# Kernel optimization log

Measured on AMD Instinct MI355X. Metric: run time of the kernel, lower is better.

Reference implementation:

```python
import jax, jax.numpy as jnp
import numpy as np

EMBED = 2048
HEADS = 16
HEAD_DIM = EMBED // HEADS


def setup_inputs() -> dict:
    key = jax.random.key(0)
    ks = jax.random.split(key, 9)
    s = 1.0 / np.sqrt(EMBED)
    inp = {"x": jax.random.normal(ks[0], (2, 2048, EMBED), dtype=jnp.float32)}
    for i, name in enumerate(["q", "k", "v", "o"]):
        inp[f"W{name}"] = jax.random.uniform(ks[1 + 2 * i], (EMBED, EMBED), dtype=jnp.float32, minval=-s, maxval=s)
        inp[f"b{name}"] = jax.random.uniform(ks[2 + 2 * i], (EMBED,), dtype=jnp.float32, minval=-s, maxval=s)
    return inp


def reference(x, Wq, bq, Wk, bk, Wv, bv, Wo, bo):
    B, S, E = x.shape
    def split_heads(t):
        return t.reshape(B, S, HEADS, HEAD_DIM).transpose(0, 2, 1, 3)  # [B,H,S,D]
    q = split_heads(x @ Wq.T + bq)
    k = split_heads(x @ Wk.T + bk)
    v = split_heads(x @ Wv.T + bv)
    scale = 1.0 / np.sqrt(HEAD_DIM)
    scores = jnp.einsum("bhqd,bhkd->bhqk", q, k) * scale  # [B,H,S,S]
    causal = jnp.tril(jnp.ones((S, S), dtype=bool))
    scores = jnp.where(causal[None, None], scores, -jnp.inf)
    attn = jax.nn.softmax(scores, axis=-1)
    out = jnp.einsum("bhqk,bhkd->bhqd", attn, v)  # [B,H,S,D]
    out = out.transpose(0, 2, 1, 3).reshape(B, S, E)
    return out @ Wo.T + bo
```

## Files before the change

kernel.cpp:

```cpp
#include <hip/hip_runtime.h>

typedef unsigned short u16;
typedef unsigned int u32;
typedef __attribute__((ext_vector_type(8))) short bf16x8;
typedef __attribute__((ext_vector_type(4))) float f32x4;

#define MFMA(a, b, c) __builtin_amdgcn_mfma_f32_16x16x32_bf16((a), (b), (c), 0, 0, 0)

__device__ inline u16 f2bf(float f) {
  u32 u = __float_as_uint(f);
  u = (u + 0x7fffu + ((u >> 16) & 1u)) >> 16;
  return (u16)u;
}

__device__ inline void gld16(u16* lds, const u16* g) {
  __builtin_amdgcn_global_load_lds((const __attribute__((address_space(1))) void*)g,
                                   (__attribute__((address_space(3))) void*)lds,
                                   16, 0, 0);
}

__global__ __launch_bounds__(256) void cvt_all(const float* __restrict__ x,
                                               const float* __restrict__ wa,
                                               const float* __restrict__ wb,
                                               const float* __restrict__ wc,
                                               const float* __restrict__ wd,
                                               uint2* __restrict__ dst) {
  int i = blockIdx.x * 256 + threadIdx.x;
  const float* s;
  int off;
  if (i < 2097152) {
    s = x; off = i;
  } else {
    int j = i - 2097152;
    int which = j >> 20;
    off = j & 1048575;
    s = (which == 0) ? wa : (which == 1) ? wb : (which == 2) ? wc : wd;
  }
  float4 f = ((const float4*)s)[off];
  u32 lo = (u32)f2bf(f.x) | ((u32)f2bf(f.y) << 16);
  u32 hi = (u32)f2bf(f.z) | ((u32)f2bf(f.w) << 16);
  dst[i] = make_uint2(lo, hi);
}

__device__ inline void gemm_core(const u16* __restrict__ A, const u16* __restrict__ W,
                                 u16* As, u16* Bs, int m0, int n0, f32x4 acc[4][4]) {
  const int K = 2048;
  const int NT = 64;
  int t = threadIdx.x, w = t >> 6, l = t & 63;
  int wr = (w >> 1) * 64, wc = (w & 1) * 64;
  int fr = l & 15, fg = l >> 4;
  int r0 = t >> 2;
  int r1 = 64 + r0;
  int c00 = (t & 3) ^ ((r0 >> 1) & 3);
  int c01 = (t & 3) ^ ((r1 >> 1) & 3);
  const u16* gA = A + (size_t)m0 * K;
  const u16* gB = W + (size_t)n0 * K;
  size_t a0 = (size_t)r0 * K + c00 * 8;
  size_t a1 = (size_t)r1 * K + c01 * 8;
#pragma unroll
  for (int p = 0; p < 2; ++p) {
    u16* sa = As + p * 4096;
    u16* sb = Bs + p * 4096;
    int kk = p * 32;
    gld16(sa + w * 512, gA + a0 + kk);
    gld16(sa + 2048 + w * 512, gA + a1 + kk);
    gld16(sb + w * 512, gB + a0 + kk);
    gld16(sb + 2048 + w * 512, gB + a1 + kk);
  }
  for (int kt = 0; kt < NT; ++kt) {
    int kt2 = (kt + 2 < NT) ? (kt + 2) : (NT - 1);
    u16* sa = As + ((kt + 2) & 3) * 4096;
    u16* sb = Bs + ((kt + 2) & 3) * 4096;
    int kk = kt2 * 32;
    gld16(sa + w * 512, gA + a0 + kk);
    gld16(sa + 2048 + w * 512, gA + a1 + kk);
    gld16(sb + w * 512, gB + a0 + kk);
    gld16(sb + 2048 + w * 512, gB + a1 + kk);
    asm volatile("s_waitcnt vmcnt(8)\n\ts_barrier" ::: "memory");
    const u16* ca = As + (kt & 3) * 4096;
    const u16* cb = Bs + (kt & 3) * 4096;
    bf16x8 af[4], bfv[4];
#pragma unroll
    for (int i = 0; i < 4; ++i) {
      int ar = wr + i * 16 + fr;
      af[i] = *(const bf16x8*)&ca[ar * 32 + ((fg ^ ((ar >> 1) & 3)) << 3)];
    }
#pragma unroll
    for (int i = 0; i < 4; ++i) {
      int br = wc + i * 16 + fr;
      bfv[i] = *(const bf16x8*)&cb[br * 32 + ((fg ^ ((br >> 1) & 3)) << 3)];
    }
    __builtin_amdgcn_s_setprio(1);
#pragma unroll
    for (int mi = 0; mi < 4; ++mi)
#pragma unroll
      for (int ni = 0; ni < 4; ++ni)
        acc[mi][ni] = MFMA(af[mi], bfv[ni], acc[mi][ni]);
    __builtin_amdgcn_s_setprio(0);
  }
}

__global__ __launch_bounds__(512, 2) void qk_gemm(
    const u16* __restrict__ X, const u16* __restrict__ Wq, const u16* __restrict__ Wk,
    const float* __restrict__ bq, const float* __restrict__ bk, u16* __restrict__ Qo,
    u16* __restrict__ Ko) {
  __shared__ __attribute__((aligned(16))) u16 As[32768];
  __shared__ __attribute__((aligned(16))) u16 Bs[32768];
  const int K = 2048, NT = 64;
  int which = blockIdx.x >> 3;
  int n0 = (blockIdx.x & 7) * 256;
  int m0 = blockIdx.y * 256;
  const u16* W = (which == 0) ? Wq : Wk;
  const float* bias = (which == 0) ? bq : bk;
  u16* out = (which == 0) ? Qo : Ko;
  float scale = (which == 0) ? 0.08838834764831845f : 1.0f;
  int t = threadIdx.x, w = t >> 6, l = t & 63;
  int wm = w >> 2, wn = w & 3;
  int fr = l & 15, fg = l >> 4;
  int r0 = t >> 2;
  int c0 = (t & 3) ^ ((r0 >> 1) & 3);
  const u16* gA = X + (size_t)m0 * K;
  const u16* gB = W + (size_t)n0 * K;
  size_t a0 = (size_t)r0 * K + c0 * 8;
  size_t a1 = a0 + (size_t)128 * K;
  f32x4 zero4 = {0.f, 0.f, 0.f, 0.f};
  f32x4 acc[8][4];
#pragma unroll
  for (int i = 0; i < 8; ++i)
#pragma unroll
    for (int j = 0; j < 4; ++j) acc[i][j] = zero4;
#pragma unroll
  for (int p = 0; p < 2; ++p) {
    u16* sa = As + p * 8192;
    u16* sb = Bs + p * 8192;
    int kk = p * 32;
    gld16(sa + w * 512, gA + a0 + kk);
    gld16(sa + 4096 + w * 512, gA + a1 + kk);
    gld16(sb + w * 512, gB + a0 + kk);
    gld16(sb + 4096 + w * 512, gB + a1 + kk);
  }
  for (int kt = 0; kt < NT; ++kt) {
    int kt2 = (kt + 2 < NT) ? (kt + 2) : (NT - 1);
    u16* sa = As + ((kt + 2) & 3) * 8192;
    u16* sb = Bs + ((kt + 2) & 3) * 8192;
    int kk = kt2 * 32;
    gld16(sa + w * 512, gA + a0 + kk);
    gld16(sa + 4096 + w * 512, gA + a1 + kk);
    gld16(sb + w * 512, gB + a0 + kk);
    gld16(sb + 4096 + w * 512, gB + a1 + kk);
    asm volatile("s_waitcnt vmcnt(8)\n\ts_barrier" ::: "memory");
    const u16* ca = As + (kt & 3) * 8192;
    const u16* cb = Bs + (kt & 3) * 8192;
    bf16x8 af[8], bfv[4];
#pragma unroll
    for (int i = 0; i < 8; ++i) {
      int ar = wm * 128 + i * 16 + fr;
      af[i] = *(const bf16x8*)&ca[ar * 32 + ((fg ^ ((ar >> 1) & 3)) << 3)];
    }
#pragma unroll
    for (int i = 0; i < 4; ++i) {
      int br = wn * 64 + i * 16 + fr;
      bfv[i] = *(const bf16x8*)&cb[br * 32 + ((fg ^ ((br >> 1) & 3)) << 3)];
    }
    __builtin_amdgcn_s_setprio(1);
#pragma unroll
    for (int mi = 0; mi < 8; ++mi)
#pragma unroll
      for (int ni = 0; ni < 4; ++ni)
        acc[mi][ni] = MFMA(af[mi], bfv[ni], acc[mi][ni]);
    __builtin_amdgcn_s_setprio(0);
  }
#pragma unroll
  for (int mi = 0; mi < 8; ++mi) {
#pragma unroll
    for (int ni = 0; ni < 4; ++ni) {
      int row = m0 + wm * 128 + mi * 16 + (l >> 4) * 4;
      int col = n0 + wn * 64 + ni * 16 + (l & 15);
      float bb = bias[col];
      int h = col >> 7, d = col & 127;
#pragma unroll
      for (int i = 0; i < 4; ++i) {
        int m = row + i;
        int b = m >> 11, s = m & 2047;
        float v = (acc[mi][ni][i] + bb) * scale;
        out[(((size_t)b * 16 + h) * 2048 + s) * 128 + d] = f2bf(v);
      }
    }
  }
}

__global__ __launch_bounds__(256, 2) void v_gemm(const u16* __restrict__ X,
                                                 const u16* __restrict__ Wv,
                                                 const float* __restrict__ bv,
                                                 u16* __restrict__ Vo) {
  __shared__ __attribute__((aligned(16))) u16 As[16384];
  __shared__ __attribute__((aligned(16))) u16 Bs[16384];
  int n0 = blockIdx.x * 128, m0 = blockIdx.y * 128;
  f32x4 zero4 = {0.f, 0.f, 0.f, 0.f};
  f32x4 acc[4][4];
#pragma unroll
  for (int i = 0; i < 4; ++i)
#pragma unroll
    for (int j = 0; j < 4; ++j) acc[i][j] = zero4;
  gemm_core(X, Wv, As, Bs, m0, n0, acc);
  int t = threadIdx.x, w = t >> 6, l = t & 63;
  int wr = (w >> 1) * 64, wc = (w & 1) * 64;
#pragma unroll
  for (int mi = 0; mi < 4; ++mi) {
#pragma unroll
    for (int ni = 0; ni < 4; ++ni) {
      int row = m0 + wr + mi * 16 + (l >> 4) * 4;
      int col = n0 + wc + ni * 16 + (l & 15);
      float bb = bv[col];
      int h = col >> 7, d = col & 127;
      int b = row >> 11, s = row & 2047;
      u32 p0 = (u32)f2bf(acc[mi][ni][0] + bb) | ((u32)f2bf(acc[mi][ni][1] + bb) << 16);
      u32 p1 = (u32)f2bf(acc[mi][ni][2] + bb) | ((u32)f2bf(acc[mi][ni][3] + bb) << 16);
      *(uint2*)&Vo[((size_t)(b * 16 + h) * 128 + d) * 2048 + s] = make_uint2(p0, p1);
    }
  }
}

__global__ __launch_bounds__(256, 2) void oproj_gemm(const u16* __restrict__ A,
                                                     const u16* __restrict__ W,
                                                     const float* __restrict__ bias,
                                                     float* __restrict__ out) {
  __shared__ __attribute__((aligned(16))) u16 As[16384];
  __shared__ __attribute__((aligned(16))) u16 Bs[16384];
  int n0 = blockIdx.x * 128, m0 = blockIdx.y * 128;
  f32x4 zero4 = {0.f, 0.f, 0.f, 0.f};
  f32x4 acc[4][4];
#pragma unroll
  for (int i = 0; i < 4; ++i)
#pragma unroll
    for (int j = 0; j < 4; ++j) acc[i][j] = zero4;
  gemm_core(A, W, As, Bs, m0, n0, acc);
  int t = threadIdx.x, w = t >> 6, l = t & 63;
  int wr = (w >> 1) * 64, wc = (w & 1) * 64;
#pragma unroll
  for (int mi = 0; mi < 4; ++mi) {
#pragma unroll
    for (int ni = 0; ni < 4; ++ni) {
      int row = m0 + wr + mi * 16 + (l >> 4) * 4;
      int col = n0 + wc + ni * 16 + (l & 15);
      float bb = bias[col];
#pragma unroll
      for (int i = 0; i < 4; ++i) out[(size_t)(row + i) * 2048 + col] = acc[mi][ni][i] + bb;
    }
  }
}

__global__ __launch_bounds__(512, 4) void attn_fwd(const u16* __restrict__ Q,
                                                   const u16* __restrict__ K,
                                                   const u16* __restrict__ Vt,
                                                   u16* __restrict__ AO) {
  __shared__ __attribute__((aligned(16))) u16 Ks[16384];
  __shared__ __attribute__((aligned(16))) u16 Vts[16384];
  __shared__ __attribute__((aligned(16))) u16 Pl[8192];
  const int D = 128;
  int b3 = blockIdx.x;
  int bh = b3 & 31;
  int xq = b3 >> 5;
  int qt = (xq < 8) ? (15 - xq) : (xq - 8);
  int t = threadIdx.x, w = t >> 6, l = t & 63, g = l >> 4, c = l & 15;
  size_t base = (size_t)bh * 2048 * 128;
  const u16* Vbh = Vt + base;
  int q0 = qt * 128;
  int qrw = q0 + w * 16;
  bf16x8 qf[4];
  {
    const u16* qp = Q + base + (size_t)(qrw + c) * D + g * 8;
#pragma unroll
    for (int ks = 0; ks < 4; ++ks) qf[ks] = *(const bf16x8*)(qp + ks * 32);
  }
  f32x4 zero4 = {0.f, 0.f, 0.f, 0.f};
  f32x4 oacc[8];
#pragma unroll
  for (int i = 0; i < 8; ++i) oacc[i] = zero4;
  f32x4 lacc = zero4;
  bf16x8 ones;
#pragma unroll
  for (int i = 0; i < 8; ++i) ones[i] = (short)0x3F80;
  float mrow[4];
#pragma unroll
  for (int i = 0; i < 4; ++i) mrow[i] = -1e30f;
  char* pw = (char*)(Pl + w * 1024);
  int ktmax = 2 * qt + 1;
#define STAGE_TILE(BUF, KV0)                                                          \
  {                                                                                   \
    _Pragma("unroll") for (int i = 0; i < 2; ++i) {                                   \
      int row = i * 32 + w * 4 + (l >> 4);                                            \
      int cc = (l & 15) ^ (row & 7);                                                  \
      gld16(Ks + (BUF)*8192 + i * 4096 + w * 512,                                     \
            K + base + (size_t)((KV0) + row) * D + cc * 8);                           \
    }                                                                                 \
    _Pragma("unroll") for (int i = 0; i < 2; ++i) {                                   \
      int vr = i * 64 + w * 8 + (l >> 3);                                             \
      int vslot = (l & 7) ^ ((l >> 3) & 7);                                           \
      gld16(Vts + (BUF)*8192 + i * 4096 + w * 512,                                    \
            Vbh + (size_t)vr * 2048 + (KV0) + vslot * 8);                             \
    }                                                                                 \
  }
  STAGE_TILE(0, 0)
  for (int kt = 0; kt <= ktmax; ++kt) {
    int kv0 = kt * 64;
    int ktn = (kt + 1 <= ktmax) ? (kt + 1) : ktmax;
    STAGE_TILE((kt + 1) & 1, ktn * 64)
    asm volatile("s_waitcnt vmcnt(4)\n\ts_barrier" ::: "memory");
    const u16* Kb = Ks + (kt & 1) * 8192;
    const u16* Vb2 = Vts + (kt & 1) * 8192;
    if (kv0 <= qrw + 15) {
      f32x4 sacc[4];
#pragma unroll
      for (int n = 0; n < 4; ++n) sacc[n] = zero4;
#pragma unroll
      for (int ks = 0; ks < 4; ++ks) {
#pragma unroll
        for (int n = 0; n < 4; ++n) {
          int row = n * 16 + c;
          bf16x8 kf = *(const bf16x8*)&Kb[row * 128 + (((ks * 4 + g) ^ (c & 7)) << 3)];
          sacc[n] = MFMA(qf[ks], kf, sacc[n]);
        }
      }
      float sc[4][4];
#pragma unroll
      for (int n = 0; n < 4; ++n)
#pragma unroll
        for (int i = 0; i < 4; ++i) sc[n][i] = sacc[n][i];
      if (kv0 + 63 > qrw) {
#pragma unroll
        for (int n = 0; n < 4; ++n) {
          int kv = kv0 + n * 16 + c;
#pragma unroll
          for (int i = 0; i < 4; ++i)
            if (kv > qrw + g * 4 + i) sc[n][i] = -1e30f;
        }
      }
      float tmax[4];
#pragma unroll
      for (int i = 0; i < 4; ++i)
        tmax[i] = fmaxf(fmaxf(sc[0][i], sc[1][i]), fmaxf(sc[2][i], sc[3][i]));
#pragma unroll
      for (int x = 1; x < 16; x <<= 1)
#pragma unroll
        for (int i = 0; i < 4; ++i) tmax[i] = fmaxf(tmax[i], __shfl_xor(tmax[i], x));
      float corr[4];
#pragma unroll
      for (int i = 0; i < 4; ++i) {
        float mn = fmaxf(mrow[i], tmax[i]);
        corr[i] = __expf(mrow[i] - mn);
        mrow[i] = mn;
      }
#pragma unroll
      for (int i = 0; i < 4; ++i) lacc[i] *= corr[i];
#pragma unroll
      for (int nf = 0; nf < 8; ++nf)
#pragma unroll
        for (int i = 0; i < 4; ++i) oacc[nf][i] *= corr[i];
      float ps[4][4];
#pragma unroll
      for (int n = 0; n < 4; ++n)
#pragma unroll
        for (int i = 0; i < 4; ++i) ps[n][i] = __expf(sc[n][i] - mrow[i]);
#pragma unroll
      for (int n = 0; n < 4; ++n)
#pragma unroll
        for (int i = 0; i < 4; ++i) {
          int row = g * 4 + i;
          *(u16*)(pw + row * 128 + ((n * 32 + c * 2) ^ ((row >> 2) << 5))) = f2bf(ps[n][i]);
        }
#pragma unroll
      for (int ks = 0; ks < 2; ++ks) {
        bf16x8 pf = *(const bf16x8*)(pw + c * 128 + ((ks * 64 + g * 16) ^ ((c >> 2) << 5)));
        lacc = MFMA(pf, ones, lacc);
#pragma unroll
        for (int nf = 0; nf < 8; ++nf) {
          bf16x8 vf = *(const bf16x8*)&Vb2[(nf * 16 + c) * 64 + (((ks * 4 + g) ^ (c & 7)) << 3)];
          oacc[nf] = MFMA(pf, vf, oacc[nf]);
        }
      }
    }
    __syncthreads();
  }
  int b = bh >> 4, h = bh & 15;
#pragma unroll
  for (int nf = 0; nf < 8; ++nf) {
    int d = h * 128 + nf * 16 + c;
#pragma unroll
    for (int i = 0; i < 4; ++i) {
      int q = qrw + g * 4 + i;
      AO[((size_t)b * 2048 + q) * 2048 + d] = f2bf(oacc[nf][i] / lacc[i]);
    }
  }
}

extern "C" void kernel_launch(void* const* d_in, const int* in_sizes, int n_in,
                              void* d_out, int out_size, void* d_ws, size_t ws_size,
                              hipStream_t stream) {
  const float* x = (const float*)d_in[0];
  const float* Wq = (const float*)d_in[1];
  const float* bq = (const float*)d_in[2];
  const float* Wk = (const float*)d_in[3];
  const float* bk = (const float*)d_in[4];
  const float* Wv = (const float*)d_in[5];
  const float* bv = (const float*)d_in[6];
  const float* Wo = (const float*)d_in[7];
  const float* bo = (const float*)d_in[8];
  float* out = (float*)d_out;

  u16* xb = (u16*)d_ws;
  u16* Wqb = xb + 8388608;
  u16* Wkb = Wqb + 4194304;
  u16* Wvb = Wkb + 4194304;
  u16* Wob = Wvb + 4194304;
  u16* Qb = Wob + 4194304;
  u16* Kb = Qb + 8388608;
  u16* Vb = Kb + 8388608;
  u16* AOb = xb;

  cvt_all<<<24576, 256, 0, stream>>>(x, Wq, Wk, Wv, Wo, (uint2*)d_ws);
  qk_gemm<<<dim3(16, 16), 512, 0, stream>>>(xb, Wqb, Wkb, bq, bk, Qb, Kb);
  v_gemm<<<dim3(16, 32), 256, 0, stream>>>(xb, Wvb, bv, Vb);
  attn_fwd<<<512, 512, 0, stream>>>(Qb, Kb, Vb, AOb);
  oproj_gemm<<<dim3(16, 32), 256, 0, stream>>>(AOb, Wob, bo, out);
}
```

Before: 257.2 us.

## Replace double-buffered K/V staging in attention with single-buffer synchronous loads

Removes the double-buffered K/V tile prefetch in the attention kernel. Each K/V tile is now loaded into a single LDS buffer between two barriers, which halves the K/V LDS footprint, and the occupancy hint in launch bounds is lowered from 4 to 3. The smaller LDS use could allow more resident blocks. In exchange, the load of the next tile no longer overlaps compute, and there is an extra barrier per iteration. Also, __syncthreads does not obviously wait on the async global_load_lds counter (vmcnt), so visibility of the loaded data may depend on what the compiler emits.

New measurement: 259.9 us. No clear change (+1.1%).

```diff
diff --git a/kernel.cpp b/kernel.cpp
--- a/kernel.cpp
+++ b/kernel.cpp
@@ -250,12 +250,12 @@
   }
 }
 
-__global__ __launch_bounds__(512, 4) void attn_fwd(const u16* __restrict__ Q,
+__global__ __launch_bounds__(512, 3) void attn_fwd(const u16* __restrict__ Q,
                                                    const u16* __restrict__ K,
                                                    const u16* __restrict__ Vt,
                                                    u16* __restrict__ AO) {
-  __shared__ __attribute__((aligned(16))) u16 Ks[16384];
-  __shared__ __attribute__((aligned(16))) u16 Vts[16384];
+  __shared__ __attribute__((aligned(16))) u16 Ks[8192];
+  __shared__ __attribute__((aligned(16))) u16 Vts[8192];
   __shared__ __attribute__((aligned(16))) u16 Pl[8192];
   const int D = 128;
   int b3 = blockIdx.x;
@@ -286,29 +286,22 @@
   for (int i = 0; i < 4; ++i) mrow[i] = -1e30f;
   char* pw = (char*)(Pl + w * 1024);
   int ktmax = 2 * qt + 1;
-#define STAGE_TILE(BUF, KV0)                                                          \
-  {                                                                                   \
-    _Pragma("unroll") for (int i = 0; i < 2; ++i) {                                   \
-      int row = i * 32 + w * 4 + (l >> 4);                                            \
-      int cc = (l & 15) ^ (row & 7);                                                  \
-      gld16(Ks + (BUF)*8192 + i * 4096 + w * 512,                                     \
-            K + base + (size_t)((KV0) + row) * D + cc * 8);                           \
-    }                                                                                 \
-    _Pragma("unroll") for (int i = 0; i < 2; ++i) {                                   \
-      int vr = i * 64 + w * 8 + (l >> 3);                                             \
-      int vslot = (l & 7) ^ ((l >> 3) & 7);                                           \
-      gld16(Vts + (BUF)*8192 + i * 4096 + w * 512,                                    \
-            Vbh + (size_t)vr * 2048 + (KV0) + vslot * 8);                             \
-    }                                                                                 \
-  }
-  STAGE_TILE(0, 0)
   for (int kt = 0; kt <= ktmax; ++kt) {
     int kv0 = kt * 64;
-    int ktn = (kt + 1 <= ktmax) ? (kt + 1) : ktmax;
-    STAGE_TILE((kt + 1) & 1, ktn * 64)
-    asm volatile("s_waitcnt vmcnt(4)\n\ts_barrier" ::: "memory");
-    const u16* Kb = Ks + (kt & 1) * 8192;
-    const u16* Vb2 = Vts + (kt & 1) * 8192;
+    __syncthreads();
+#pragma unroll
+    for (int i = 0; i < 2; ++i) {
+      int row = i * 32 + w * 4 + (l >> 4);
+      int cc = (l & 15) ^ (row & 7);
+      gld16(Ks + i * 4096 + w * 512, K + base + (size_t)(kv0 + row) * D + cc * 8);
+    }
+#pragma unroll
+    for (int i = 0; i < 2; ++i) {
+      int vr = i * 64 + w * 8 + (l >> 3);
+      int vslot = (l & 7) ^ ((l >> 3) & 7);
+      gld16(Vts + i * 4096 + w * 512, Vbh + (size_t)vr * 2048 + kv0 + vslot * 8);
+    }
+    __syncthreads();
     if (kv0 <= qrw + 15) {
       f32x4 sacc[4];
 #pragma unroll
@@ -318,7 +311,7 @@
 #pragma unroll
         for (int n = 0; n < 4; ++n) {
           int row = n * 16 + c;
-          bf16x8 kf = *(const bf16x8*)&Kb[row * 128 + (((ks * 4 + g) ^ (c & 7)) << 3)];
+          bf16x8 kf = *(const bf16x8*)&Ks[row * 128 + (((ks * 4 + g) ^ (c & 7)) << 3)];
           sacc[n] = MFMA(qf[ks], kf, sacc[n]);
         }
       }
@@ -375,12 +368,11 @@
         lacc = MFMA(pf, ones, lacc);
 #pragma unroll
         for (int nf = 0; nf < 8; ++nf) {
-          bf16x8 vf = *(const bf16x8*)&Vb2[(nf * 16 + c) * 64 + (((ks * 4 + g) ^ (c & 7)) << 3)];
+          bf16x8 vf = *(const bf16x8*)&Vts[(nf * 16 + c) * 64 + (((ks * 4 + g) ^ (c & 7)) << 3)];
           oacc[nf] = MFMA(pf, vf, oacc[nf]);
         }
       }
     }
-    __syncthreads();
   }
   int b = bh >> 4, h = bh & 15;
 #pragma unroll
```
